# Kernel optimization log

Measured on AMD Instinct MI355X. Metric: run time of the kernel, lower is better.

The kernel has to match this reference:

```python
import jax, jax.numpy as jnp
import numpy as np

DT = 0.001
BATCH, INPUT_SIZE, HIDDEN_SIZE, T = 32, 16384, 1024, 10


def setup_inputs() -> dict:
    key = jax.random.key(0)
    k1, k2, k3 = jax.random.split(key, 3)
    input_spikes = (jax.random.uniform(k1, (BATCH, INPUT_SIZE, T)) < 0.1).astype(jnp.float32)
    weight = jax.random.normal(k2, (INPUT_SIZE, HIDDEN_SIZE), dtype=jnp.float32) * 0.1
    synaptic_strength = jnp.ones((INPUT_SIZE, HIDDEN_SIZE), jnp.float32)
    threshold = jnp.ones((HIDDEN_SIZE,), jnp.float32)  # threshold_init = 1.0
    firing_rate_estimate = jnp.zeros((HIDDEN_SIZE,), jnp.float32)
    return {
        "input_spikes": input_spikes,
        "weight": weight,
        "synaptic_strength": synaptic_strength,
        "threshold": threshold,
        "firing_rate_estimate": firing_rate_estimate,
        "tau_mem": jnp.float32(0.02),
        "tau_syn": jnp.float32(0.005),
        "target_rate": jnp.float32(0.1),
        "homeostatic_lr": jnp.float32(0.001),
        "time_steps": T,
    }


def reference(input_spikes, weight, synaptic_strength, threshold,
              firing_rate_estimate, tau_mem, tau_syn, target_rate,
              homeostatic_lr, time_steps):
    # input_spikes: [B, I, T]; eval mode (no stochastic STDP branch)
    B = input_spikes.shape[0]
    H = threshold.shape[0]
    alpha_mem = jnp.exp(-DT / tau_mem)
    alpha_syn = jnp.exp(-DT / tau_syn)
    # precompute the per-step weighted input once: [T, B, H]
    w_eff = weight * synaptic_strength
    weighted = jnp.einsum('bit,ih->tbh', input_spikes[..., :time_steps], w_eff)

    def step(carry, w_in):
        v, i, fre, thr = carry
        i = alpha_syn * i + w_in
        v = alpha_mem * v + i
        spikes = (v >= thr[None, :]).astype(v.dtype)
        v = v - spikes * thr[None, :]  # reset_mode='subtract'
        spike_rate = spikes.mean(axis=0)
        fre = 0.99 * fre + 0.01 * spike_rate
        thr = thr + homeostatic_lr * (fre - target_rate)  # homeostatic adaptation
        diag = (v.mean(), spike_rate.mean(), thr.mean())
        return (v, i, fre, thr), (spikes, diag)

    init = (jnp.zeros((B, H), input_spikes.dtype),
            jnp.zeros((B, H), input_spikes.dtype),
            firing_rate_estimate, threshold)
    _, (spikes_tbh, (mem_means, rate_means, thr_means)) = jax.lax.scan(step, init, weighted)
    output_spikes = jnp.transpose(spikes_tbh, (1, 2, 0))  # [B, H, T]
    return output_spikes, mem_means, rate_means, thr_means
```

## Files before the change

### kernel.cpp

```cpp
#include <hip/hip_runtime.h>
#include <stdint.h>

#define B_ 32
#define I_ 16384
#define H_ 1024
#define T_ 10
#define M_ 320
#define NW 64
#define BK 32
#define SCAN_BLOCKS 256

typedef __attribute__((ext_vector_type(8))) short short8;
typedef __attribute__((ext_vector_type(4))) float f32x4;
typedef __attribute__((ext_vector_type(2))) float f32x2;
typedef __attribute__((ext_vector_type(4))) unsigned int u32x4;

__global__ __launch_bounds__(256) void pack_s(const float* __restrict__ spikes,
                                              uint16_t* __restrict__ Sbf) {
  __shared__ __align__(16) uint16_t tile[M_ * 40];
  const int i0 = blockIdx.x * 32;
#pragma unroll
  for (int p = 0; p < 10; p++) {
    int e = p * 256 + threadIdx.x;
    int b = e / 80;
    int r = e - b * 80;
    f32x4 val = *(const f32x4*)&spikes[(size_t)b * (I_ * T_) + (size_t)i0 * T_ + r * 4];
#pragma unroll
    for (int j = 0; j < 4; j++) {
      int pos = r * 4 + j;
      int il = pos / 10;
      int t = pos - il * 10;
      float f = (j == 0) ? val.x : (j == 1) ? val.y : (j == 2) ? val.z : val.w;
      union { float f; unsigned int u; } cv; cv.f = f;
      tile[(t * 32 + b) * 40 + il] = (uint16_t)(cv.u >> 16);
    }
  }
  __syncthreads();
#pragma unroll
  for (int p = 0; p < 5; p++) {
    int e = p * 256 + threadIdx.x;
    int m = e >> 2, il8 = e & 3;
    u32x4 w = *(const u32x4*)&tile[m * 40 + il8 * 8];
    *(u32x4*)&Sbf[(size_t)m * I_ + i0 + il8 * 8] = w;
  }
}

__global__ __launch_bounds__(640, 5) void gemm(const uint16_t* __restrict__ Sbf,
                                               const float* __restrict__ Wg,
                                               const float* __restrict__ Sg,
                                               float* __restrict__ partial,
                                               int kchunk, int KS) {
  __shared__ __align__(16) uint16_t WhiL[2][NW * 40];
  __shared__ __align__(16) uint16_t WloL[2][NW * 40];

  const int ks = blockIdx.x % KS;
  const int nt = blockIdx.x / KS;
  const int nbase = nt * NW;
  const int tid = threadIdx.x;
  const int lane = tid & 63, wid = tid >> 6;
  const int quad = lane >> 4, l15 = lane & 15;

  const int stages = kchunk >> 5;
  const int kofs = ks * kchunk;

  const uint16_t* aptr0 = Sbf + (size_t)(wid * 32 + l15) * I_ + quad * 8;
  const uint16_t* aptr1 = aptr0 + (size_t)16 * I_;

  const int wn = tid & 63;
  const int wko = (tid >> 6) & 3;

  f32x4 acc[2][4];
#pragma unroll
  for (int a = 0; a < 2; a++)
#pragma unroll
    for (int b = 0; b < 4; b++) acc[a][b] = f32x4{0.f, 0.f, 0.f, 0.f};

  u32x4 af[2];
  float wpre[8], spre[8];

#define BAR()                                                               \
  do {                                                                      \
    asm volatile("s_waitcnt lgkmcnt(0)" ::: "memory");                      \
    __builtin_amdgcn_s_barrier();                                           \
    __builtin_amdgcn_sched_barrier(0);                                      \
  } while (0)

#define PACK_W(pn)                                                          \
  if (tid < 256) {                                                          \
    unsigned int hw[4], lw[4];                                              \
    _Pragma("unroll")                                                       \
    for (int j2 = 0; j2 < 4; j2++) {                                        \
      unsigned int hh[2], ll[2];                                            \
      _Pragma("unroll")                                                     \
      for (int e = 0; e < 2; e++) {                                         \
        float p = wpre[j2 * 2 + e] * spre[j2 * 2 + e];                      \
        union { float f; unsigned int u; } cv; cv.f = p;                    \
        unsigned int hb = (cv.u + 0x7FFFu + ((cv.u >> 16) & 1u)) >> 16;     \
        union { unsigned int u; float f; } hv; hv.u = hb << 16;             \
        float lo = p - hv.f;                                                \
        union { float f; unsigned int u; } cl; cl.f = lo;                   \
        unsigned int lb = (cl.u + 0x7FFFu + ((cl.u >> 16) & 1u)) >> 16;     \
        hh[e] = hb; ll[e] = lb;                                             \
      }                                                                     \
      hw[j2] = hh[0] | (hh[1] << 16);                                       \
      lw[j2] = ll[0] | (ll[1] << 16);                                       \
    }                                                                       \
    int wofs = wn * 40 + wko * 8;                                           \
    *(u32x4*)&WhiL[pn][wofs] = u32x4{hw[0], hw[1], hw[2], hw[3]};           \
    *(u32x4*)&WloL[pn][wofs] = u32x4{lw[0], lw[1], lw[2], lw[3]};           \
  }

#define LOAD_W(kb)                                                          \
  if (tid < 256) {                                                          \
    _Pragma("unroll")                                                       \
    for (int j = 0; j < 8; j++) {                                           \
      size_t g = (size_t)((kb) + wko * 8 + j) * H_ + nbase + wn;            \
      wpre[j] = Wg[g]; spre[j] = Sg[g];                                     \
    }                                                                       \
  }

#define ISSUE_A(kb)                                                         \
  {                                                                         \
    af[0] = *(const u32x4*)(aptr0 + (kb));                                  \
    af[1] = *(const u32x4*)(aptr1 + (kb));                                  \
  }

#define COMPUTE(pc)                                                         \
  {                                                                         \
    short8 a0 = __builtin_bit_cast(short8, af[0]);                          \
    short8 a1 = __builtin_bit_cast(short8, af[1]);                          \
    _Pragma("unroll")                                                       \
    for (int tn = 0; tn < 4; ++tn) {                                        \
      int n = tn * 16 + l15;                                                \
      short8 bhi = *(const short8*)&WhiL[pc][n * 40 + quad * 8];            \
      short8 blo = *(const short8*)&WloL[pc][n * 40 + quad * 8];            \
      acc[0][tn] = __builtin_amdgcn_mfma_f32_16x16x32_bf16(a0, bhi, acc[0][tn], 0, 0, 0); \
      acc[0][tn] = __builtin_amdgcn_mfma_f32_16x16x32_bf16(a0, blo, acc[0][tn], 0, 0, 0); \
      acc[1][tn] = __builtin_amdgcn_mfma_f32_16x16x32_bf16(a1, bhi, acc[1][tn], 0, 0, 0); \
      acc[1][tn] = __builtin_amdgcn_mfma_f32_16x16x32_bf16(a1, blo, acc[1][tn], 0, 0, 0); \
    }                                                                       \
  }

  LOAD_W(kofs);
  ISSUE_A(kofs);
  PACK_W(0);
  if (stages > 1) LOAD_W(kofs + BK);
  BAR();

  for (int s = 0; s < stages; ++s) {
    COMPUTE(s & 1);
    if (s + 1 < stages) {
      ISSUE_A(kofs + (s + 1) * BK);
      PACK_W((s + 1) & 1);
      if (s + 2 < stages) LOAD_W(kofs + (s + 2) * BK);
      BAR();
    }
  }

#pragma unroll
  for (int tm = 0; tm < 2; tm++)
#pragma unroll
    for (int tn = 0; tn < 4; tn++) {
      int mrow = wid * 32 + tm * 16 + quad * 4;
      int ncol = nbase + tn * 16 + l15;
      float* dst = partial + ((size_t)ks * M_ + mrow) * H_ + ncol;
      dst[0 * H_] = acc[tm][tn].x;
      dst[1 * H_] = acc[tm][tn].y;
      dst[2 * H_] = acc[tm][tn].z;
      dst[3 * H_] = acc[tm][tn].w;
    }
#undef PACK_W
#undef LOAD_W
#undef ISSUE_A
#undef COMPUTE
#undef BAR
}

__global__ __launch_bounds__(256) void reduce_w(const float* __restrict__ partial,
                                                float* __restrict__ weighted,
                                                int KS) {
  int j = (blockIdx.x * 256 + threadIdx.x) * 4;
  f32x4 s = f32x4{0.f, 0.f, 0.f, 0.f};
  if (KS == 32) {
#pragma unroll
    for (int k = 0; k < 32; k++) {
      f32x4 p = *(const f32x4*)&partial[(size_t)k * (M_ * H_) + j];
      s += p;
    }
  } else {
    for (int k = 0; k < KS; k++) {
      f32x4 p = *(const f32x4*)&partial[(size_t)k * (M_ * H_) + j];
      s += p;
    }
  }
  *(f32x4*)&weighted[j] = s;
}

__global__ __launch_bounds__(128) void scan(const float* __restrict__ weighted,
                                            const float* __restrict__ threshold,
                                            const float* __restrict__ fre0,
                                            const float* __restrict__ p_tau_mem,
                                            const float* __restrict__ p_tau_syn,
                                            const float* __restrict__ p_target,
                                            const float* __restrict__ p_lr,
                                            float* __restrict__ out,
                                            float* __restrict__ dpart) {
  const int tid = threadIdx.x;
  const int lane = tid & 63;
  const int wv = tid >> 6;
  const int b = lane & 31;
  const int hg = lane >> 5;
  const int h = blockIdx.x * 4 + wv * 2 + hg;

  const float alpha_mem = expf(-0.001f / p_tau_mem[0]);
  const float alpha_syn = expf(-0.001f / p_tau_syn[0]);
  const float target = p_target[0], lr = p_lr[0];

  float win[T_];
#pragma unroll
  for (int t = 0; t < T_; t++)
    win[t] = weighted[(size_t)(t * 32 + b) * H_ + h];

  float fre = fre0[h];
  float thr = threshold[h];
  float v = 0.f, isyn = 0.f;
  float spk[T_], dv[T_], dr[T_], dtt[T_];

#pragma unroll
  for (int t = 0; t < T_; t++) {
    isyn = alpha_syn * isyn + win[t];
    v = alpha_mem * v + isyn;
    float spike = (v >= thr) ? 1.f : 0.f;
    v -= spike * thr;
    spk[t] = spike;
    float r = spike;
    r += __shfl_xor(r, 1);
    r += __shfl_xor(r, 2);
    r += __shfl_xor(r, 4);
    r += __shfl_xor(r, 8);
    r += __shfl_xor(r, 16);
    float rate = r * (1.f / 32.f);
    fre = 0.99f * fre + 0.01f * rate;
    thr = thr + lr * (fre - target);
    float vv = v;
#pragma unroll
    for (int off = 1; off <= 32; off <<= 1) vv += __shfl_xor(vv, off);
    float r2 = r + __shfl_xor(r, 32);
    float t2 = thr + __shfl_xor(thr, 32);
    dv[t] = vv;
    dr[t] = r2 * (1.f / 32.f);
    dtt[t] = t2;
  }

  {
    float* o = out + (size_t)b * (H_ * T_) + (size_t)h * T_;
#pragma unroll
    for (int p = 0; p < 5; p++)
      *(f32x2*)&o[p * 2] = f32x2{spk[p * 2], spk[p * 2 + 1]};
  }

  __shared__ float dl[2][30];
  if (lane == 0) {
#pragma unroll
    for (int t = 0; t < T_; t++) {
      dl[wv][t] = dv[t];
      dl[wv][10 + t] = dr[t];
      dl[wv][20 + t] = dtt[t];
    }
  }
  __syncthreads();
  if (tid < 30) dpart[(size_t)blockIdx.x * 30 + tid] = dl[0][tid] + dl[1][tid];
}

__global__ __launch_bounds__(128) void reduce_d(const float* __restrict__ dpart,
                                                float* __restrict__ out) {
  __shared__ float accl[4][32];
  const int s = threadIdx.x >> 5;
  const int c = threadIdx.x & 31;
  float sum = 0.f;
  if (c < 30) {
    for (int k = s * 64; k < s * 64 + 64; k++)
      sum += dpart[(size_t)k * 30 + c];
  }
  accl[s][c] = sum;
  __syncthreads();
  if (threadIdx.x < 30) {
    float tot = accl[0][threadIdx.x] + accl[1][threadIdx.x] +
                accl[2][threadIdx.x] + accl[3][threadIdx.x];
    float scale = (threadIdx.x < 10) ? (1.f / 32768.f) : (1.f / 1024.f);
    out[327680 + threadIdx.x] = tot * scale;
  }
}

extern "C" void kernel_launch(void* const* d_in, const int* in_sizes, int n_in,
                              void* d_out, int out_size, void* d_ws, size_t ws_size,
                              hipStream_t stream) {
  const float* spikes    = (const float*)d_in[0];
  const float* weight    = (const float*)d_in[1];
  const float* strength  = (const float*)d_in[2];
  const float* threshold = (const float*)d_in[3];
  const float* fre0      = (const float*)d_in[4];
  const float* tau_mem   = (const float*)d_in[5];
  const float* tau_syn   = (const float*)d_in[6];
  const float* target    = (const float*)d_in[7];
  const float* lr        = (const float*)d_in[8];
  float* out = (float*)d_out;

  const size_t sbf_bytes = (size_t)M_ * I_ * 2;
  const size_t slice     = (size_t)M_ * H_ * 4;
  const size_t wt_bytes  = (size_t)M_ * H_ * 4;
  const size_t dp_bytes  = (size_t)SCAN_BLOCKS * 30 * 4;
  int KS = 32;
  while (KS > 1 &&
         sbf_bytes + (size_t)KS * slice + wt_bytes + dp_bytes > ws_size)
    KS >>= 1;

  uint16_t* Sbf   = (uint16_t*)d_ws;
  float* partial  = (float*)((char*)d_ws + sbf_bytes);
  float* weighted = (float*)((char*)d_ws + sbf_bytes + (size_t)KS * slice);
  float* dpart    = (float*)((char*)d_ws + sbf_bytes + (size_t)KS * slice + wt_bytes);

  pack_s<<<I_ / 32, 256, 0, stream>>>(spikes, Sbf);
  gemm<<<(H_ / NW) * KS, 640, 0, stream>>>(Sbf, weight, strength, partial,
                                           I_ / KS, KS);
  reduce_w<<<(M_ * H_) / 1024, 256, 0, stream>>>(partial, weighted, KS);
  scan<<<SCAN_BLOCKS, 128, 0, stream>>>(weighted, threshold, fre0, tau_mem,
                                        tau_syn, target, lr, out, dpart);
  reduce_d<<<1, 128, 0, stream>>>(dpart, out);
}
```

Before: 211.5 us.

## Stream weight tiles into LDS with async global_load_lds triple buffering

Replaces per-thread register prefetch of weight and synaptic-strength tiles with direct global-to-LDS async loads into a 3-deep raw buffer. The bf16 hi/lo split packing now reads from LDS and runs one stage ahead, ahead of the MFMA compute. Loads are issued three stages in advance and gated with explicit vmcnt waits. The aim is to hide global latency and free registers, at the cost of extra LDS footprint, which may lower occupancy, and fragile hand-counted waitcnt logic.

```diff
diff --git a/kernel.cpp b/kernel.cpp
--- a/kernel.cpp
+++ b/kernel.cpp
@@ -8,6 +8,7 @@
 #define M_ 320
 #define NW 64
 #define BK 32
+#define RB 3
 #define SCAN_BLOCKS 256
 
 typedef __attribute__((ext_vector_type(8))) short short8;
@@ -50,6 +51,8 @@
                                                const float* __restrict__ Sg,
                                                float* __restrict__ partial,
                                                int kchunk, int KS) {
+  __shared__ __align__(16) float rawW[RB][BK * NW];
+  __shared__ __align__(16) float rawS[RB][BK * NW];
   __shared__ __align__(16) uint16_t WhiL[2][NW * 40];
   __shared__ __align__(16) uint16_t WloL[2][NW * 40];
 
@@ -66,6 +69,8 @@
   const uint16_t* aptr0 = Sbf + (size_t)(wid * 32 + l15) * I_ + quad * 8;
   const uint16_t* aptr1 = aptr0 + (size_t)16 * I_;
 
+  const size_t gstage = (size_t)(wid * 4 + (lane >> 4)) * H_ + nbase + (lane & 15) * 4;
+
   const int wn = tid & 63;
   const int wko = (tid >> 6) & 3;
 
@@ -76,24 +81,40 @@
     for (int b = 0; b < 4; b++) acc[a][b] = f32x4{0.f, 0.f, 0.f, 0.f};
 
   u32x4 af[2];
-  float wpre[8], spre[8];
-
-#define BAR()                                                               \
-  do {                                                                      \
-    asm volatile("s_waitcnt lgkmcnt(0)" ::: "memory");                      \
-    __builtin_amdgcn_s_barrier();                                           \
-    __builtin_amdgcn_sched_barrier(0);                                      \
-  } while (0)
-
-#define PACK_W(pn)                                                          \
+
+#define ISSUE_W(sidx)                                                       \
+  if (tid < 512) {                                                          \
+    const int _rb = (sidx) % RB;                                            \
+    const float* gw = Wg + (size_t)(kofs + (sidx) * BK) * H_ + gstage;      \
+    const float* gs = Sg + (size_t)(kofs + (sidx) * BK) * H_ + gstage;      \
+    __builtin_amdgcn_global_load_lds(                                       \
+        (const __attribute__((address_space(1))) void*)gw,                  \
+        (__attribute__((address_space(3))) void*)&rawW[_rb][wid * 256],     \
+        16, 0, 0);                                                          \
+    __builtin_amdgcn_global_load_lds(                                       \
+        (const __attribute__((address_space(1))) void*)gs,                  \
+        (__attribute__((address_space(3))) void*)&rawS[_rb][wid * 256],     \
+        16, 0, 0);                                                          \
+  }
+
+#define ISSUE_A(kb)                                                         \
+  {                                                                         \
+    af[0] = *(const u32x4*)(aptr0 + (kb));                                  \
+    af[1] = *(const u32x4*)(aptr1 + (kb));                                  \
+  }
+
+#define PACK_W(sidx)                                                        \
   if (tid < 256) {                                                          \
+    const int _rb = (sidx) % RB;                                            \
+    const int _pn = (sidx) & 1;                                             \
     unsigned int hw[4], lw[4];                                              \
     _Pragma("unroll")                                                       \
     for (int j2 = 0; j2 < 4; j2++) {                                        \
       unsigned int hh[2], ll[2];                                            \
       _Pragma("unroll")                                                     \
       for (int e = 0; e < 2; e++) {                                         \
-        float p = wpre[j2 * 2 + e] * spre[j2 * 2 + e];                      \
+        int r = wko * 8 + j2 * 2 + e;                                       \
+        float p = rawW[_rb][r * 64 + wn] * rawS[_rb][r * 64 + wn];          \
         union { float f; unsigned int u; } cv; cv.f = p;                    \
         unsigned int hb = (cv.u + 0x7FFFu + ((cv.u >> 16) & 1u)) >> 16;     \
         union { unsigned int u; float f; } hv; hv.u = hb << 16;             \
@@ -106,23 +127,8 @@
       lw[j2] = ll[0] | (ll[1] << 16);                                       \
     }                                                                       \
     int wofs = wn * 40 + wko * 8;                                           \
-    *(u32x4*)&WhiL[pn][wofs] = u32x4{hw[0], hw[1], hw[2], hw[3]};           \
-    *(u32x4*)&WloL[pn][wofs] = u32x4{lw[0], lw[1], lw[2], lw[3]};           \
-  }
-
-#define LOAD_W(kb)                                                          \
-  if (tid < 256) {                                                          \
-    _Pragma("unroll")                                                       \
-    for (int j = 0; j < 8; j++) {                                           \
-      size_t g = (size_t)((kb) + wko * 8 + j) * H_ + nbase + wn;            \
-      wpre[j] = Wg[g]; spre[j] = Sg[g];                                     \
-    }                                                                       \
-  }
-
-#define ISSUE_A(kb)                                                         \
-  {                                                                         \
-    af[0] = *(const u32x4*)(aptr0 + (kb));                                  \
-    af[1] = *(const u32x4*)(aptr1 + (kb));                                  \
+    *(u32x4*)&WhiL[_pn][wofs] = u32x4{hw[0], hw[1], hw[2], hw[3]};          \
+    *(u32x4*)&WloL[_pn][wofs] = u32x4{lw[0], lw[1], lw[2], lw[3]};          \
   }
 
 #define COMPUTE(pc)                                                         \
@@ -141,19 +147,35 @@
     }                                                                       \
   }
 
-  LOAD_W(kofs);
+  ISSUE_W(0);
+  ISSUE_W(1);
   ISSUE_A(kofs);
+  ISSUE_W(2);
+  if (tid < 512) asm volatile("s_waitcnt vmcnt(6)" ::: "memory");
+  __builtin_amdgcn_s_barrier();
+  __builtin_amdgcn_sched_barrier(0);
   PACK_W(0);
-  if (stages > 1) LOAD_W(kofs + BK);
-  BAR();
+  if (tid < 512) asm volatile("s_waitcnt vmcnt(4)" ::: "memory");
+  asm volatile("s_waitcnt lgkmcnt(0)" ::: "memory");
+  __builtin_amdgcn_s_barrier();
+  __builtin_amdgcn_sched_barrier(0);
 
   for (int s = 0; s < stages; ++s) {
+    if (s + 1 < stages) PACK_W(s + 1);
+    __builtin_amdgcn_sched_barrier(0);
     COMPUTE(s & 1);
+    __builtin_amdgcn_sched_barrier(0);
     if (s + 1 < stages) {
       ISSUE_A(kofs + (s + 1) * BK);
-      PACK_W((s + 1) & 1);
-      if (s + 2 < stages) LOAD_W(kofs + (s + 2) * BK);
-      BAR();
+      if (s + 3 < stages) {
+        ISSUE_W(s + 3);
+        if (tid < 512) asm volatile("s_waitcnt vmcnt(4)" ::: "memory");
+      } else {
+        if (tid < 512) asm volatile("s_waitcnt vmcnt(2)" ::: "memory");
+      }
+      asm volatile("s_waitcnt lgkmcnt(0)" ::: "memory");
+      __builtin_amdgcn_s_barrier();
+      __builtin_amdgcn_sched_barrier(0);
     }
   }
 
@@ -170,10 +192,9 @@
       dst[3 * H_] = acc[tm][tn].w;
     }
 #undef PACK_W
-#undef LOAD_W
+#undef ISSUE_W
 #undef ISSUE_A
 #undef COMPUTE
-#undef BAR
 }
 
 __global__ __launch_bounds__(256) void reduce_w(const float* __restrict__ partial,
```

Measured after the change: 222.8 us. 1.05x slower.
